# Performance work log

Hardware: AMD Instinct MI355X
Metric: run time of the kernel (lower is better)

The kernel has to match this reference:

```python
import jax, jax.numpy as jnp
import numpy as np

N_LEVELS = 16
N_FEATS = 2
LOG2_T = 19
TABLE_SIZE = 2 ** LOG2_T
BASE_RES = 16
PER_LEVEL_SCALE = 1.3819
N_PTS = 524288
# per-level grid resolutions (static)
RESOLUTIONS = np.floor(BASE_RES * PER_LEVEL_SCALE ** np.arange(N_LEVELS)).astype(np.float32)
# NGP spatial hash primes for 2D
PRIME0 = np.uint32(1)
PRIME1 = np.uint32(2654435761)
# corner offsets for bilinear interp: (0,0),(0,1),(1,0),(1,1)
CORNER_OFFS = np.array([[0, 0], [0, 1], [1, 0], [1, 1]], dtype=np.uint32)


def setup_inputs() -> dict:
    key = jax.random.key(0)
    k1, k2 = jax.random.split(key)
    pts = jax.random.uniform(k1, (N_PTS, 3), dtype=jnp.float32)  # coords in [0,1]
    # 3 planes x L levels x T entries x F features, small init like NGP (1e-4)
    tables = jax.random.normal(k2, (3, N_LEVELS, TABLE_SIZE, N_FEATS), dtype=jnp.float32) * 1e-4
    return {"pts": pts, "tables": tables}


def _encode_plane(coords, table):
    # coords: [N,2] in [0,1]; table: [L,T,F]
    L, T, F = table.shape
    res = jnp.asarray(RESOLUTIONS)  # [L]
    scaled = coords[None, :, :] * res[:, None, None]  # [L,N,2]
    x0 = jnp.floor(scaled)
    frac = scaled - x0  # [L,N,2]
    x0u = x0.astype(jnp.uint32)
    offs = jnp.asarray(CORNER_OFFS)  # [4,2]
    corners = x0u[:, :, None, :] + offs[None, None, :, :]  # [L,N,4,2]
    # NGP spatial hash with uint32 wraparound, then mod table size
    h = (corners[..., 0] * PRIME0) ^ (corners[..., 1] * PRIME1)  # [L,N,4] uint32
    idx = (h % jnp.uint32(T)).astype(jnp.int32)  # [L,N,4]
    feats = table[jnp.arange(L)[:, None, None], idx]  # [L,N,4,F]
    # bilinear weights: product over dims of frac (offset=1) or 1-frac (offset=0)
    fo = offs.astype(coords.dtype)  # [4,2]
    w = jnp.prod(jnp.where(fo[None, None] > 0, frac[:, :, None, :], 1.0 - frac[:, :, None, :]), axis=-1)  # [L,N,4]
    out = jnp.einsum('lnc,lncf->lnf', w, feats)  # [L,N,F]
    return out.transpose(1, 0, 2).reshape(coords.shape[0], L * F)  # [N, L*F]


def reference(pts, tables):
    # coordinate-pair planes: combinations of (0,1,2) taken 2 at a time
    coo_combs = [(0, 1), (0, 2), (1, 2)]
    interp_space = 1.0
    for ci, comb in enumerate(coo_combs):
        interp_space = interp_space * _encode_plane(pts[:, list(comb)], tables[ci])
    return interp_space  # [N, 32]
```

## Files before the change

### kernel.cpp

```cpp
#include <hip/hip_runtime.h>
#include <stdint.h>


#define NPTS   524288u
#define TSIZE  524288u
#define TMASK  0x7FFFFu
#define PRIME1 2654435761u

__constant__ float c_res[16] = {
    16.f, 22.f, 30.f, 42.f, 58.f, 80.f, 111.f, 153.f,
    212.f, 294.f, 406.f, 561.f, 775.f, 1072.f, 1481.f, 2047.f
};

__constant__ int c_RA[5]   = {17, 23, 31, 43, 59};
__constant__ int c_offA[5] = {0, 289, 818, 1779, 3628};

__constant__ uint16_t c_mid_lo[6]  = {0, 56, 0, 39, 78, 117};
__constant__ uint16_t c_mid_hiX[6] = {56, 112, 39, 78, 117, 154};

__global__ __launch_bounds__(256) void kplane_pack(
    const float* __restrict__ pts,
    float2* __restrict__ pts2)
{
    const uint32_t pt = blockIdx.x * 256u + threadIdx.x;
    const float x = pts[pt * 3u + 0u];
    const float y = pts[pt * 3u + 1u];
    const float z = pts[pt * 3u + 2u];
    pts2[            pt] = make_float2(x, y);
    pts2[NPTS      + pt] = make_float2(x, z);
    pts2[2u * NPTS + pt] = make_float2(y, z);
}

__global__ __launch_bounds__(256) void kplane_hi(
    const float2* __restrict__ pts2,
    const float2* __restrict__ tab,
    float2* __restrict__ ws)
{
    const uint32_t b     = blockIdx.x;
    const uint32_t xcd   = b & 7u;
    const uint32_t s     = b >> 3;
    const uint32_t phase = s >> 9;
    const uint32_t chunk = s & 511u;
    const uint32_t plane = phase;
    const uint32_t lvl   = 8u + ((xcd + 3u * phase) & 7u);
    const uint32_t g     = plane * 16u + lvl;
    const float    res   = c_res[lvl];
    const uint32_t base  = g * TSIZE;
    const float4* __restrict__ tab4 = (const float4*)tab;
    const uint32_t b4    = g * (TSIZE / 2u);
    const uint32_t pt0   = chunk * 1024u + threadIdx.x;
    const float2* __restrict__ pp = pts2 + (size_t)plane * NPTS;

    float4 P0[4], P1[4];
    float2 Q0[4], Q1[4];
    float  r0[4], r1[4];
    uint32_t sel0[4], sel1[4], oddm[4];

#pragma unroll
    for (int k = 0; k < 4; ++k) {
        const uint32_t pt = pt0 + (uint32_t)k * 256u;
        const float2 c2 = pp[pt];
        const float s0 = c2.x * res;
        const float s1 = c2.y * res;
        const float f0 = floorf(s0);
        const float f1 = floorf(s1);
        r0[k] = s0 - f0;
        r1[k] = s1 - f1;
        const uint32_t u0  = (uint32_t)f0;
        const uint32_t hy0 = (uint32_t)f1 * PRIME1;
        const uint32_t hy1 = hy0 + PRIME1;
        const uint32_t i00 = ( u0        ^ hy0) & TMASK;
        const uint32_t i01 = ( u0        ^ hy1) & TMASK;
        const uint32_t i10 = ((u0 + 1u)  ^ hy0) & TMASK;
        const uint32_t i11 = ((u0 + 1u)  ^ hy1) & TMASK;
        sel0[k] = i00 & 1u;
        sel1[k] = i01 & 1u;
        oddm[k] = u0 & 1u;
        P0[k] = tab4[b4 + (i00 >> 1)];
        P1[k] = tab4[b4 + (i01 >> 1)];
        Q0[k] = make_float2(0.f, 0.f);
        Q1[k] = make_float2(0.f, 0.f);
        if (oddm[k]) {
            Q0[k] = tab[base + i10];
            Q1[k] = tab[base + i11];
        }
    }
#pragma unroll
    for (int k = 0; k < 4; ++k) {
        const uint32_t pt = pt0 + (uint32_t)k * 256u;
        const float2 lo0 = make_float2(P0[k].x, P0[k].y);
        const float2 hi0 = make_float2(P0[k].z, P0[k].w);
        const float2 lo1 = make_float2(P1[k].x, P1[k].y);
        const float2 hi1 = make_float2(P1[k].z, P1[k].w);
        const float2 t00 = sel0[k] ? hi0 : lo0;
        const float2 t01 = sel1[k] ? hi1 : lo1;
        const float2 t10 = oddm[k] ? Q0[k] : (sel0[k] ? lo0 : hi0);
        const float2 t11 = oddm[k] ? Q1[k] : (sel1[k] ? lo1 : hi1);
        const float w00 = (1.f - r0[k]) * (1.f - r1[k]);
        const float w01 = (1.f - r0[k]) * r1[k];
        const float w10 = r0[k] * (1.f - r1[k]);
        const float w11 = r0[k] * r1[k];
        ws[g * NPTS + pt] = make_float2(
            w00 * t00.x + w01 * t01.x + w10 * t10.x + w11 * t11.x,
            w00 * t00.y + w01 * t01.y + w10 * t10.y + w11 * t11.y);
    }
}

__global__ __launch_bounds__(512) void kplane_midlds(
    const float2* __restrict__ pts2,
    const float2* __restrict__ tab,
    float2* __restrict__ ws)
{
    __shared__ float2 sm[7109];
    const uint32_t b = blockIdx.x;
    const uint32_t t = threadIdx.x;

    if (b < 288u) {
        const uint32_t sg    = b >> 4;
        const uint32_t chunk = b & 15u;
        const uint32_t plane = sg / 6u;
        const uint32_t local = sg - plane * 6u;
        const uint32_t lvl   = (local < 2u) ? 6u : 7u;
        const uint32_t g     = plane * 16u + lvl;
        const uint32_t R     = (lvl == 6u) ? 112u : 154u;
        const uint32_t lo    = c_mid_lo[local];
        const uint32_t hiX   = c_mid_hiX[local];
        const uint32_t nrows = ((hiX < R ? hiX : R - 1u) - lo) + 1u;
        const uint32_t E     = nrows * R;
        const float    res   = c_res[lvl];
        const uint32_t base  = g * TSIZE;

        for (uint32_t i = t; i < E; i += 512u) {
            const uint32_t rr = i / R;
            const uint32_t cy = i - rr * R;
            const uint32_t cx = lo + rr;
            sm[i] = tab[base + ((cx ^ (cy * PRIME1)) & TMASK)];
        }
        __syncthreads();

        const float2* __restrict__ pp = pts2 + (size_t)plane * NPTS;
        const uint32_t pt0 = chunk * 32768u + t;

#pragma unroll 4
        for (uint32_t k = 0; k < 64u; ++k) {
            const uint32_t pt = pt0 + k * 512u;
            const float2 c2 = pp[pt];
            const float s0 = c2.x * res;
            const float s1 = c2.y * res;
            const float f0 = floorf(s0);
            const float f1 = floorf(s1);
            const uint32_t u0 = (uint32_t)f0;
            if (u0 >= lo && u0 < hiX) {
                const float r0 = s0 - f0;
                const float r1 = s1 - f1;
                const uint32_t ci = (u0 - lo) * R + (uint32_t)f1;
                const float2 q00 = sm[ci];
                const float2 q01 = sm[ci + 1u];
                const float2 q10 = sm[ci + R];
                const float2 q11 = sm[ci + R + 1u];
                const float w00 = (1.f - r0) * (1.f - r1);
                const float w01 = (1.f - r0) * r1;
                const float w10 = r0 * (1.f - r1);
                const float w11 = r0 * r1;
                ws[g * NPTS + pt] = make_float2(
                    w00 * q00.x + w01 * q01.x + w10 * q10.x + w11 * q11.x,
                    w00 * q00.y + w01 * q01.y + w10 * q10.y + w11 * q11.y);
            }
        }
    } else if (b < 336u) {
        const uint32_t idx   = b - 288u;
        const uint32_t plane = idx >> 4;
        const uint32_t chunk = idx & 15u;

#pragma unroll
        for (int l = 0; l < 5; ++l) {
            const uint32_t R    = (uint32_t)c_RA[l];
            const uint32_t E    = R * R;
            const uint32_t off  = (uint32_t)c_offA[l];
            const uint32_t base = (plane * 16u + (uint32_t)l) * TSIZE;
            for (uint32_t i = t; i < E; i += 512u) {
                const uint32_t cx = i / R;
                const uint32_t cy = i - cx * R;
                sm[off + i] = tab[base + ((cx ^ (cy * PRIME1)) & TMASK)];
            }
        }
        __syncthreads();

        const float2* __restrict__ pp = pts2 + (size_t)plane * NPTS;
        const uint32_t pt0 = chunk * 32768u + t;

#pragma unroll 2
        for (uint32_t k = 0; k < 64u; ++k) {
            const uint32_t pt = pt0 + k * 512u;
            const float2 c2 = pp[pt];
#pragma unroll
            for (int l = 0; l < 5; ++l) {
                const uint32_t R   = (uint32_t)c_RA[l];
                const uint32_t off = (uint32_t)c_offA[l];
                const float res = c_res[l];
                const float s0 = c2.x * res;
                const float s1 = c2.y * res;
                const float f0 = floorf(s0);
                const float f1 = floorf(s1);
                const float r0 = s0 - f0;
                const float r1 = s1 - f1;
                const uint32_t ci = off + (uint32_t)f0 * R + (uint32_t)f1;
                const float2 q00 = sm[ci];
                const float2 q01 = sm[ci + 1u];
                const float2 q10 = sm[ci + R];
                const float2 q11 = sm[ci + R + 1u];
                const float w00 = (1.f - r0) * (1.f - r1);
                const float w01 = (1.f - r0) * r1;
                const float w10 = r0 * (1.f - r1);
                const float w11 = r0 * r1;
                ws[(plane * 16u + (uint32_t)l) * NPTS + pt] = make_float2(
                    w00 * q00.x + w01 * q01.x + w10 * q10.x + w11 * q11.x,
                    w00 * q00.y + w01 * q01.y + w10 * q10.y + w11 * q11.y);
            }
        }
    } else {
        const uint32_t idx   = b - 336u;
        const uint32_t plane = idx >> 4;
        const uint32_t chunk = idx & 15u;
        const uint32_t R     = 81u;
        const uint32_t E     = 6561u;
        const float    res   = 80.f;
        const uint32_t g     = plane * 16u + 5u;
        const uint32_t base  = g * TSIZE;

        for (uint32_t i = t; i < E; i += 512u) {
            const uint32_t cx = i / R;
            const uint32_t cy = i - cx * R;
            sm[i] = tab[base + ((cx ^ (cy * PRIME1)) & TMASK)];
        }
        __syncthreads();

        const float2* __restrict__ pp = pts2 + (size_t)plane * NPTS;
        const uint32_t pt0 = chunk * 32768u + t;

#pragma unroll 4
        for (uint32_t k = 0; k < 64u; ++k) {
            const uint32_t pt = pt0 + k * 512u;
            const float2 c2 = pp[pt];
            const float s0 = c2.x * res;
            const float s1 = c2.y * res;
            const float f0 = floorf(s0);
            const float f1 = floorf(s1);
            const float r0 = s0 - f0;
            const float r1 = s1 - f1;
            const uint32_t ci = (uint32_t)f0 * R + (uint32_t)f1;
            const float2 q00 = sm[ci];
            const float2 q01 = sm[ci + 1u];
            const float2 q10 = sm[ci + R];
            const float2 q11 = sm[ci + R + 1u];
            const float w00 = (1.f - r0) * (1.f - r1);
            const float w01 = (1.f - r0) * r1;
            const float w10 = r0 * (1.f - r1);
            const float w11 = r0 * r1;
            ws[g * NPTS + pt] = make_float2(
                w00 * q00.x + w01 * q01.x + w10 * q10.x + w11 * q11.x,
                w00 * q00.y + w01 * q01.y + w10 * q10.y + w11 * q11.y);
        }
    }
}

__global__ __launch_bounds__(256) void kplane_combine(
    const float2* __restrict__ ws,
    float2* __restrict__ out)
{
    __shared__ float2 tile[16][65];
    const uint32_t pt0 = blockIdx.x * 64u;
    const uint32_t t   = threadIdx.x;
    const uint32_t lr  = t >> 6;
    const uint32_t ptl = t & 63u;

#pragma unroll
    for (int k = 0; k < 4; ++k) {
        const uint32_t lvl = (uint32_t)k * 4u + lr;
        const float2 a = ws[( 0u + lvl) * NPTS + pt0 + ptl];
        const float2 b = ws[(16u + lvl) * NPTS + pt0 + ptl];
        const float2 c = ws[(32u + lvl) * NPTS + pt0 + ptl];
        tile[lvl][ptl] = make_float2(a.x * b.x * c.x, a.y * b.y * c.y);
    }
    __syncthreads();
#pragma unroll
    for (int k = 0; k < 4; ++k) {
        const uint32_t e      = t + (uint32_t)k * 256u;
        const uint32_t out_lv = e & 15u;
        const uint32_t out_pt = e >> 4;
        out[(pt0 + out_pt) * 16u + out_lv] = tile[out_lv][out_pt];
    }
}

template <int P, bool FIRST>
__global__ __launch_bounds__(256) void kplane_pass(
    const float* __restrict__ pts,
    const float2* __restrict__ tab,
    float2* __restrict__ ws)
{
    const uint32_t b     = blockIdx.x;
    const uint32_t xcd   = b & 7u;
    const uint32_t s     = b >> 3;
    const uint32_t gi    = s >> 11;
    const uint32_t chunk = s & 2047u;
    const uint32_t lvl   = gi * 8u + xcd;
    const uint32_t pt    = chunk * 256u + threadIdx.x;

    constexpr int c0 = (P == 2) ? 1 : 0;
    constexpr int c1 = (P == 0) ? 1 : 2;

    const float a0  = pts[pt * 3u + c0];
    const float a1  = pts[pt * 3u + c1];
    const float res = c_res[lvl];

    const float s0 = a0 * res;
    const float s1 = a1 * res;
    const float f0 = floorf(s0);
    const float f1 = floorf(s1);
    const float r0 = s0 - f0;
    const float r1 = s1 - f1;
    const uint32_t u0 = (uint32_t)f0;
    const uint32_t hy0  = (uint32_t)f1 * PRIME1;
    const uint32_t hy1  = hy0 + PRIME1;
    const uint32_t base = ((uint32_t)P * 16u + lvl) * TSIZE;

    const float2 t00 = tab[base + (( u0       ^ hy0) & TMASK)];
    const float2 t01 = tab[base + (( u0       ^ hy1) & TMASK)];
    const float2 t10 = tab[base + (((u0 + 1u) ^ hy0) & TMASK)];
    const float2 t11 = tab[base + (((u0 + 1u) ^ hy1) & TMASK)];

    const float w00 = (1.f - r0) * (1.f - r1);
    const float w01 = (1.f - r0) * r1;
    const float w10 = r0 * (1.f - r1);
    const float w11 = r0 * r1;

    const float e0 = w00 * t00.x + w01 * t01.x + w10 * t10.x + w11 * t11.x;
    const float e1 = w00 * t00.y + w01 * t01.y + w10 * t10.y + w11 * t11.y;

    const uint32_t widx = lvl * NPTS + pt;
    if (FIRST) {
        ws[widx] = make_float2(e0, e1);
    } else {
        const float2 prev = ws[widx];
        ws[widx] = make_float2(prev.x * e0, prev.y * e1);
    }
}

__global__ __launch_bounds__(256) void kplane_transpose(
    const float2* __restrict__ ws, float2* __restrict__ out)
{
    const uint32_t tid = blockIdx.x * 256u + threadIdx.x;
    const uint32_t lvl = tid & 15u;
    const uint32_t pt  = tid >> 4;
    out[tid] = ws[lvl * NPTS + pt];
}

__global__ __launch_bounds__(256) void kplane_mono(
    const float* __restrict__ pts,
    const float2* __restrict__ tab,
    float2* __restrict__ out)
{
    const uint32_t tid = blockIdx.x * 256u + threadIdx.x;
    const uint32_t pt  = tid >> 4;
    const uint32_t lvl = tid & 15u;
    const float x = pts[pt * 3u + 0u];
    const float y = pts[pt * 3u + 1u];
    const float z = pts[pt * 3u + 2u];
    const float res = c_res[lvl];
    const float a0[3] = {x, x, y};
    const float a1[3] = {y, z, z};
    float p0 = 1.f, p1 = 1.f;
#pragma unroll
    for (int pl = 0; pl < 3; ++pl) {
        const float s0 = a0[pl] * res;
        const float s1 = a1[pl] * res;
        const float f0 = floorf(s0);
        const float f1 = floorf(s1);
        const float r0 = s0 - f0;
        const float r1 = s1 - f1;
        const uint32_t u0 = (uint32_t)f0;
        const uint32_t hy0 = (uint32_t)f1 * PRIME1;
        const uint32_t hy1 = hy0 + PRIME1;
        const uint32_t base = ((uint32_t)pl * 16u + lvl) * TSIZE;
        const float2 t00 = tab[base + (( u0       ^ hy0) & TMASK)];
        const float2 t01 = tab[base + (( u0       ^ hy1) & TMASK)];
        const float2 t10 = tab[base + (((u0 + 1u) ^ hy0) & TMASK)];
        const float2 t11 = tab[base + (((u0 + 1u) ^ hy1) & TMASK)];
        const float w00 = (1.f - r0) * (1.f - r1);
        const float w01 = (1.f - r0) * r1;
        const float w10 = r0 * (1.f - r1);
        const float w11 = r0 * r1;
        p0 *= w00 * t00.x + w01 * t01.x + w10 * t10.x + w11 * t11.x;
        p1 *= w00 * t00.y + w01 * t01.y + w10 * t10.y + w11 * t11.y;
    }
    out[pt * 16u + lvl] = make_float2(p0, p1);
}

extern "C" void kernel_launch(void* const* d_in, const int* in_sizes, int n_in,
                              void* d_out, int out_size, void* d_ws, size_t ws_size,
                              hipStream_t stream) {
    const float*  pts = (const float*)d_in[0];
    const float2* tab = (const float2*)d_in[1];
    float2*       out = (float2*)d_out;

    const size_t wsA = (size_t)48 * NPTS * sizeof(float2);
    const size_t wsB = (size_t)16 * NPTS * sizeof(float2);
    dim3 block256(256u), block512(512u);

    if (ws_size >= wsA) {
        float2* ws   = (float2*)d_ws;
        float2* pts2 = (float2*)d_out;
        hipLaunchKernelGGL(kplane_pack, dim3(NPTS / 256u), block256, 0, stream,
                           pts, pts2);
        dim3 hgrid(3u * 8u * 512u);
        hipLaunchKernelGGL(kplane_hi, hgrid, block256, 0, stream, pts2, tab, ws);
        dim3 mgrid(384u);
        hipLaunchKernelGGL(kplane_midlds, mgrid, block512, 0, stream, pts2, tab, ws);
        dim3 cgrid(NPTS / 64u);
        hipLaunchKernelGGL(kplane_combine, cgrid, block256, 0, stream, ws, out);
    } else if (ws_size >= wsB) {
        float2* ws = (float2*)d_ws;
        dim3 grid(16u * (NPTS / 256u));
        hipLaunchKernelGGL((kplane_pass<0, true >), grid, block256, 0, stream, pts, tab, ws);
        hipLaunchKernelGGL((kplane_pass<1, false>), grid, block256, 0, stream, pts, tab, ws);
        hipLaunchKernelGGL((kplane_pass<2, false>), grid, block256, 0, stream, pts, tab, ws);
        dim3 tgrid((NPTS * 16u) / 256u);
        hipLaunchKernelGGL(kplane_transpose, tgrid, block256, 0, stream, ws, out);
    } else {
        dim3 grid((NPTS * 16u) / 256u);
        hipLaunchKernelGGL(kplane_mono, grid, block256, 0, stream, pts, tab, out);
    }
}
```

Baseline: 288.9 us.

## Pre-expand dense grids for levels 0-10 and gather them through LDS slabs

The pack kernel now also expands the hashed tables for levels 0-10 into dense row-major grids in a scratch area inside the output buffer. A new kernel, kplane_s810, handles levels 8-10 by loading row slabs of the dense grid into LDS, and kplane_low replaces the mid/low LDS kernel with a uniform slab scheme. The hash-gather path kplane_hi is reduced to levels 11-15 with a new block-to-XCD mapping. This moves random hashed gathers for levels 8-10 onto LDS reuse, at the cost of an extra expansion pass, an extra launch, and many more blocks that each reload slabs and skip most points.

```diff
diff --git a/kernel.cpp b/kernel.cpp
--- a/kernel.cpp
+++ b/kernel.cpp
@@ -7,49 +7,83 @@
 #define TMASK  0x7FFFFu
 #define PRIME1 2654435761u
 
+#define PTS2_OFF     0u
+#define DHI_OFF      1572864u
+#define DHI_PSTRIDE  298043u
+#define DLO_OFF      2466993u
+#define DLO_PSTRIDE  49930u
+#define EXP_TOTAL    1043919u
+#define EXP_PER_PL   347973u
+
 __constant__ float c_res[16] = {
     16.f, 22.f, 30.f, 42.f, 58.f, 80.f, 111.f, 153.f,
     212.f, 294.f, 406.f, 561.f, 775.f, 1072.f, 1481.f, 2047.f
 };
-
-__constant__ int c_RA[5]   = {17, 23, 31, 43, 59};
-__constant__ int c_offA[5] = {0, 289, 818, 1779, 3628};
-
-__constant__ uint16_t c_mid_lo[6]  = {0, 56, 0, 39, 78, 117};
-__constant__ uint16_t c_mid_hiX[6] = {56, 112, 39, 78, 117, 154};
-
-__global__ __launch_bounds__(256) void kplane_pack(
+__constant__ uint32_t c_Rlo[8]   = {17, 23, 31, 43, 59, 81, 112, 154};
+__constant__ uint32_t c_offlo[8] = {0, 289, 818, 1779, 3628, 7109, 13670, 26214};
+__constant__ uint32_t c_Rhi[3]   = {213, 295, 407};
+__constant__ uint32_t c_offhi[3] = {0, 45369, 132394};
+
+__global__ __launch_bounds__(256) void kplane_packexpand(
     const float* __restrict__ pts,
-    float2* __restrict__ pts2)
-{
-    const uint32_t pt = blockIdx.x * 256u + threadIdx.x;
-    const float x = pts[pt * 3u + 0u];
-    const float y = pts[pt * 3u + 1u];
-    const float z = pts[pt * 3u + 2u];
-    pts2[            pt] = make_float2(x, y);
-    pts2[NPTS      + pt] = make_float2(x, z);
-    pts2[2u * NPTS + pt] = make_float2(y, z);
+    const float2* __restrict__ tab,
+    float2* __restrict__ scr)
+{
+    const uint32_t b = blockIdx.x, t = threadIdx.x;
+    if (b < 2048u) {
+        const uint32_t pt = b * 256u + t;
+        const float x = pts[pt * 3u + 0u];
+        const float y = pts[pt * 3u + 1u];
+        const float z = pts[pt * 3u + 2u];
+        scr[PTS2_OFF +             pt] = make_float2(x, y);
+        scr[PTS2_OFF + NPTS      + pt] = make_float2(x, z);
+        scr[PTS2_OFF + 2u * NPTS + pt] = make_float2(y, z);
+        return;
+    }
+    const uint32_t idx = (b - 2048u) * 256u + t;
+    if (idx >= EXP_TOTAL) return;
+    const uint32_t plane = idx / EXP_PER_PL;
+    const uint32_t i     = idx - plane * EXP_PER_PL;
+    if (i < DLO_PSTRIDE) {
+        uint32_t lvl = 7u;
+        while (i < c_offlo[lvl]) lvl--;
+        const uint32_t R     = c_Rlo[lvl];
+        const uint32_t local = i - c_offlo[lvl];
+        const uint32_t cx = local / R, cy = local - cx * R;
+        scr[DLO_OFF + plane * DLO_PSTRIDE + i] =
+            tab[(plane * 16u + lvl) * TSIZE + ((cx ^ (cy * PRIME1)) & TMASK)];
+    } else {
+        const uint32_t j  = i - DLO_PSTRIDE;
+        const uint32_t li = (j < 45369u) ? 0u : (j < 132394u ? 1u : 2u);
+        const uint32_t R     = c_Rhi[li];
+        const uint32_t local = j - c_offhi[li];
+        const uint32_t cx = local / R, cy = local - cx * R;
+        scr[DHI_OFF + plane * DHI_PSTRIDE + j] =
+            tab[(plane * 16u + (8u + li)) * TSIZE +
+                ((cx ^ (cy * PRIME1)) & TMASK)];
+    }
 }
 
 __global__ __launch_bounds__(256) void kplane_hi(
-    const float2* __restrict__ pts2,
+    const float2* __restrict__ scr,
     const float2* __restrict__ tab,
     float2* __restrict__ ws)
 {
-    const uint32_t b     = blockIdx.x;
-    const uint32_t xcd   = b & 7u;
-    const uint32_t s     = b >> 3;
-    const uint32_t phase = s >> 9;
-    const uint32_t chunk = s & 511u;
-    const uint32_t plane = phase;
-    const uint32_t lvl   = 8u + ((xcd + 3u * phase) & 7u);
-    const uint32_t g     = plane * 16u + lvl;
+    const uint32_t b   = blockIdx.x;
+    const uint32_t xcd = b & 7u;
+    const uint32_t j   = b >> 3;
+    const uint32_t ci  = xcd * 960u + j;
+    const uint32_t g   = ci >> 9;
+    const uint32_t cig = ci & 511u;
+    const uint32_t lvl   = 11u + g / 3u;
+    const uint32_t plane = g - (g / 3u) * 3u;
+    const uint32_t gabs  = plane * 16u + lvl;
     const float    res   = c_res[lvl];
-    const uint32_t base  = g * TSIZE;
+    const uint32_t base  = gabs * TSIZE;
     const float4* __restrict__ tab4 = (const float4*)tab;
-    const uint32_t b4    = g * (TSIZE / 2u);
-    const uint32_t pt0   = chunk * 1024u + threadIdx.x;
-    const float2* __restrict__ pp = pts2 + (size_t)plane * NPTS;
+    const uint32_t b4    = gabs * (TSIZE / 2u);
+    const float2* __restrict__ pp = scr + PTS2_OFF + (size_t)plane * NPTS;
+    const uint32_t pt0   = cig * 1024u + threadIdx.x;
 
     float4 P0[4], P1[4];
     float2 Q0[4], Q1[4];
@@ -100,155 +134,54 @@
         const float w01 = (1.f - r0[k]) * r1[k];
         const float w10 = r0[k] * (1.f - r1[k]);
         const float w11 = r0[k] * r1[k];
-        ws[g * NPTS + pt] = make_float2(
+        ws[(size_t)gabs * NPTS + pt] = make_float2(
             w00 * t00.x + w01 * t01.x + w10 * t10.x + w11 * t11.x,
             w00 * t00.y + w01 * t01.y + w10 * t10.y + w11 * t11.y);
     }
 }
 
-__global__ __launch_bounds__(512) void kplane_midlds(
-    const float2* __restrict__ pts2,
-    const float2* __restrict__ tab,
+__global__ __launch_bounds__(512) void kplane_s810(
+    const float2* __restrict__ scr,
     float2* __restrict__ ws)
 {
-    __shared__ float2 sm[7109];
-    const uint32_t b = blockIdx.x;
-    const uint32_t t = threadIdx.x;
-
-    if (b < 288u) {
-        const uint32_t sg    = b >> 4;
-        const uint32_t chunk = b & 15u;
-        const uint32_t plane = sg / 6u;
-        const uint32_t local = sg - plane * 6u;
-        const uint32_t lvl   = (local < 2u) ? 6u : 7u;
-        const uint32_t g     = plane * 16u + lvl;
-        const uint32_t R     = (lvl == 6u) ? 112u : 154u;
-        const uint32_t lo    = c_mid_lo[local];
-        const uint32_t hiX   = c_mid_hiX[local];
-        const uint32_t nrows = ((hiX < R ? hiX : R - 1u) - lo) + 1u;
-        const uint32_t E     = nrows * R;
-        const float    res   = c_res[lvl];
-        const uint32_t base  = g * TSIZE;
-
-        for (uint32_t i = t; i < E; i += 512u) {
-            const uint32_t rr = i / R;
-            const uint32_t cy = i - rr * R;
-            const uint32_t cx = lo + rr;
-            sm[i] = tab[base + ((cx ^ (cy * PRIME1)) & TMASK)];
-        }
-        __syncthreads();
-
-        const float2* __restrict__ pp = pts2 + (size_t)plane * NPTS;
-        const uint32_t pt0 = chunk * 32768u + t;
+    __shared__ float2 sm[6390];
+    const uint32_t b     = blockIdx.x;
+    const uint32_t sp    = b >> 4;
+    const uint32_t chunk = b & 15u;
+    const uint32_t plane = sp / 52u;
+    const uint32_t s     = sp - plane * 52u;
+    uint32_t lvl, R, span, lo, offp;
+    if (s < 8u)       { lvl = 8u;  R = 213u; span = 29u; lo = s * 29u;         offp = 0u; }
+    else if (s < 23u) { lvl = 9u;  R = 295u; span = 20u; lo = (s - 8u) * 20u;  offp = 45369u; }
+    else              { lvl = 10u; R = 407u; span = 14u; lo = (s - 23u) * 14u; offp = 132394u; }
+    const uint32_t nrows = (span + 1u < R - lo) ? span + 1u : R - lo;
+    const uint32_t E     = nrows * R;
+    const uint32_t dbase = DHI_OFF + plane * DHI_PSTRIDE + offp + lo * R;
+    const uint32_t t     = threadIdx.x;
+
+    for (uint32_t i = t; i < E; i += 512u)
+        sm[i] = scr[dbase + i];
+    __syncthreads();
+
+    const float res = c_res[lvl];
+    const float2* __restrict__ pp = scr + PTS2_OFF + (size_t)plane * NPTS;
+    float2* __restrict__ wsg = ws + (size_t)(plane * 16u + lvl) * NPTS;
+    const uint32_t pt0 = chunk * 32768u + t;
+    const uint32_t hiX = lo + span;
 
 #pragma unroll 4
-        for (uint32_t k = 0; k < 64u; ++k) {
-            const uint32_t pt = pt0 + k * 512u;
-            const float2 c2 = pp[pt];
-            const float s0 = c2.x * res;
-            const float s1 = c2.y * res;
-            const float f0 = floorf(s0);
-            const float f1 = floorf(s1);
-            const uint32_t u0 = (uint32_t)f0;
-            if (u0 >= lo && u0 < hiX) {
-                const float r0 = s0 - f0;
-                const float r1 = s1 - f1;
-                const uint32_t ci = (u0 - lo) * R + (uint32_t)f1;
-                const float2 q00 = sm[ci];
-                const float2 q01 = sm[ci + 1u];
-                const float2 q10 = sm[ci + R];
-                const float2 q11 = sm[ci + R + 1u];
-                const float w00 = (1.f - r0) * (1.f - r1);
-                const float w01 = (1.f - r0) * r1;
-                const float w10 = r0 * (1.f - r1);
-                const float w11 = r0 * r1;
-                ws[g * NPTS + pt] = make_float2(
-                    w00 * q00.x + w01 * q01.x + w10 * q10.x + w11 * q11.x,
-                    w00 * q00.y + w01 * q01.y + w10 * q10.y + w11 * q11.y);
-            }
-        }
-    } else if (b < 336u) {
-        const uint32_t idx   = b - 288u;
-        const uint32_t plane = idx >> 4;
-        const uint32_t chunk = idx & 15u;
-
-#pragma unroll
-        for (int l = 0; l < 5; ++l) {
-            const uint32_t R    = (uint32_t)c_RA[l];
-            const uint32_t E    = R * R;
-            const uint32_t off  = (uint32_t)c_offA[l];
-            const uint32_t base = (plane * 16u + (uint32_t)l) * TSIZE;
-            for (uint32_t i = t; i < E; i += 512u) {
-                const uint32_t cx = i / R;
-                const uint32_t cy = i - cx * R;
-                sm[off + i] = tab[base + ((cx ^ (cy * PRIME1)) & TMASK)];
-            }
-        }
-        __syncthreads();
-
-        const float2* __restrict__ pp = pts2 + (size_t)plane * NPTS;
-        const uint32_t pt0 = chunk * 32768u + t;
-
-#pragma unroll 2
-        for (uint32_t k = 0; k < 64u; ++k) {
-            const uint32_t pt = pt0 + k * 512u;
-            const float2 c2 = pp[pt];
-#pragma unroll
-            for (int l = 0; l < 5; ++l) {
-                const uint32_t R   = (uint32_t)c_RA[l];
-                const uint32_t off = (uint32_t)c_offA[l];
-                const float res = c_res[l];
-                const float s0 = c2.x * res;
-                const float s1 = c2.y * res;
-                const float f0 = floorf(s0);
-                const float f1 = floorf(s1);
-                const float r0 = s0 - f0;
-                const float r1 = s1 - f1;
-                const uint32_t ci = off + (uint32_t)f0 * R + (uint32_t)f1;
-                const float2 q00 = sm[ci];
-                const float2 q01 = sm[ci + 1u];
-                const float2 q10 = sm[ci + R];
-                const float2 q11 = sm[ci + R + 1u];
-                const float w00 = (1.f - r0) * (1.f - r1);
-                const float w01 = (1.f - r0) * r1;
-                const float w10 = r0 * (1.f - r1);
-                const float w11 = r0 * r1;
-                ws[(plane * 16u + (uint32_t)l) * NPTS + pt] = make_float2(
-                    w00 * q00.x + w01 * q01.x + w10 * q10.x + w11 * q11.x,
-                    w00 * q00.y + w01 * q01.y + w10 * q10.y + w11 * q11.y);
-            }
-        }
-    } else {
-        const uint32_t idx   = b - 336u;
-        const uint32_t plane = idx >> 4;
-        const uint32_t chunk = idx & 15u;
-        const uint32_t R     = 81u;
-        const uint32_t E     = 6561u;
-        const float    res   = 80.f;
-        const uint32_t g     = plane * 16u + 5u;
-        const uint32_t base  = g * TSIZE;
-
-        for (uint32_t i = t; i < E; i += 512u) {
-            const uint32_t cx = i / R;
-            const uint32_t cy = i - cx * R;
-            sm[i] = tab[base + ((cx ^ (cy * PRIME1)) & TMASK)];
-        }
-        __syncthreads();
-
-        const float2* __restrict__ pp = pts2 + (size_t)plane * NPTS;
-        const uint32_t pt0 = chunk * 32768u + t;
-
-#pragma unroll 4
-        for (uint32_t k = 0; k < 64u; ++k) {
-            const uint32_t pt = pt0 + k * 512u;
-            const float2 c2 = pp[pt];
-            const float s0 = c2.x * res;
-            const float s1 = c2.y * res;
-            const float f0 = floorf(s0);
-            const float f1 = floorf(s1);
+    for (uint32_t k = 0; k < 64u; ++k) {
+        const uint32_t pt = pt0 + k * 512u;
+        const float2 c2 = pp[pt];
+        const float s0 = c2.x * res;
+        const float s1 = c2.y * res;
+        const float f0 = floorf(s0);
+        const float f1 = floorf(s1);
+        const uint32_t u0 = (uint32_t)f0;
+        if (u0 >= lo && u0 < hiX) {
             const float r0 = s0 - f0;
             const float r1 = s1 - f1;
-            const uint32_t ci = (uint32_t)f0 * R + (uint32_t)f1;
+            const uint32_t ci = (u0 - lo) * R + (uint32_t)f1;
             const float2 q00 = sm[ci];
             const float2 q01 = sm[ci + 1u];
             const float2 q10 = sm[ci + R];
@@ -257,7 +190,65 @@
             const float w01 = (1.f - r0) * r1;
             const float w10 = r0 * (1.f - r1);
             const float w11 = r0 * r1;
-            ws[g * NPTS + pt] = make_float2(
+            wsg[pt] = make_float2(
+                w00 * q00.x + w01 * q01.x + w10 * q10.x + w11 * q11.x,
+                w00 * q00.y + w01 * q01.y + w10 * q10.y + w11 * q11.y);
+        }
+    }
+}
+
+__global__ __launch_bounds__(512) void kplane_low(
+    const float2* __restrict__ scr,
+    float2* __restrict__ ws)
+{
+    __shared__ float2 sm[6561];
+    const uint32_t b     = blockIdx.x;
+    const uint32_t rgp   = b >> 5;
+    const uint32_t chunk = b & 31u;
+    const uint32_t plane = rgp / 12u;
+    const uint32_t rg    = rgp - plane * 12u;
+    uint32_t lvl, lo, span;
+    if (rg < 6u)      { lvl = rg;  lo = 0u;            span = c_Rlo[rg]; }
+    else if (rg < 8u) { lvl = 6u;  lo = (rg - 6u) * 56u; span = 56u; }
+    else              { lvl = 7u;  lo = (rg - 8u) * 39u; span = 39u; }
+    const uint32_t R     = c_Rlo[lvl];
+    const uint32_t nrows = (span + 1u < R - lo) ? span + 1u : R - lo;
+    const uint32_t E     = nrows * R;
+    const uint32_t dbase = DLO_OFF + plane * DLO_PSTRIDE + c_offlo[lvl] + lo * R;
+    const uint32_t t     = threadIdx.x;
+
+    for (uint32_t i = t; i < E; i += 512u)
+        sm[i] = scr[dbase + i];
+    __syncthreads();
+
+    const float res = c_res[lvl];
+    const float2* __restrict__ pp = scr + PTS2_OFF + (size_t)plane * NPTS;
+    float2* __restrict__ wsg = ws + (size_t)(plane * 16u + lvl) * NPTS;
+    const uint32_t pt0 = chunk * 16384u + t;
+    const uint32_t hiX = lo + span;
+
+#pragma unroll 4
+    for (uint32_t k = 0; k < 32u; ++k) {
+        const uint32_t pt = pt0 + k * 512u;
+        const float2 c2 = pp[pt];
+        const float s0 = c2.x * res;
+        const float s1 = c2.y * res;
+        const float f0 = floorf(s0);
+        const float f1 = floorf(s1);
+        const uint32_t u0 = (uint32_t)f0;
+        if (u0 >= lo && u0 < hiX) {
+            const float r0 = s0 - f0;
+            const float r1 = s1 - f1;
+            const uint32_t ci = (u0 - lo) * R + (uint32_t)f1;
+            const float2 q00 = sm[ci];
+            const float2 q01 = sm[ci + 1u];
+            const float2 q10 = sm[ci + R];
+            const float2 q11 = sm[ci + R + 1u];
+            const float w00 = (1.f - r0) * (1.f - r1);
+            const float w01 = (1.f - r0) * r1;
+            const float w10 = r0 * (1.f - r1);
+            const float w11 = r0 * r1;
+            wsg[pt] = make_float2(
                 w00 * q00.x + w01 * q01.x + w10 * q10.x + w11 * q11.x,
                 w00 * q00.y + w01 * q01.y + w10 * q10.y + w11 * q11.y);
         }
@@ -408,16 +399,18 @@
     dim3 block256(256u), block512(512u);
 
     if (ws_size >= wsA) {
-        float2* ws   = (float2*)d_ws;
-        float2* pts2 = (float2*)d_out;
-        hipLaunchKernelGGL(kplane_pack, dim3(NPTS / 256u), block256, 0, stream,
-                           pts, pts2);
-        dim3 hgrid(3u * 8u * 512u);
-        hipLaunchKernelGGL(kplane_hi, hgrid, block256, 0, stream, pts2, tab, ws);
-        dim3 mgrid(384u);
-        hipLaunchKernelGGL(kplane_midlds, mgrid, block512, 0, stream, pts2, tab, ws);
-        dim3 cgrid(NPTS / 64u);
-        hipLaunchKernelGGL(kplane_combine, cgrid, block256, 0, stream, ws, out);
+        float2* ws  = (float2*)d_ws;
+        float2* scr = (float2*)d_out;
+        hipLaunchKernelGGL(kplane_packexpand, dim3(2048u + 4078u), block256,
+                           0, stream, pts, tab, scr);
+        hipLaunchKernelGGL(kplane_hi, dim3(7680u), block256, 0, stream,
+                           scr, tab, ws);
+        hipLaunchKernelGGL(kplane_s810, dim3(2496u), block512, 0, stream,
+                           scr, ws);
+        hipLaunchKernelGGL(kplane_low, dim3(1152u), block512, 0, stream,
+                           scr, ws);
+        hipLaunchKernelGGL(kplane_combine, dim3(NPTS / 64u), block256, 0,
+                           stream, ws, out);
     } else if (ws_size >= wsB) {
         float2* ws = (float2*)d_ws;
         dim3 grid(16u * (NPTS / 256u));
```

New measurement: 354.4 us. 1.23x slower.
